# Kernel tuning notes

Hardware: AMD Instinct MI355X
Metric: run time of the kernel (lower is better)

The kernel has to match this reference:

```python
import jax, jax.numpy as jnp
import numpy as np

HOPS = 3  # max_hops; C has HOPS+1 tables

def setup_inputs() -> dict:
    key = jax.random.key(0)
    k1, k2, k3 = jax.random.split(key, 3)
    B, M, S, V, D = 32, 512, 10, 32000, 128
    story = jax.random.randint(k1, (B, M, S), 0, V)
    hidden = jax.random.normal(k2, (B, 1, D), dtype=jnp.float32)
    # hop+1 embedding tables, initialized N(0, 0.1) like the torch module
    C = 0.1 * jax.random.normal(k3, (HOPS + 1, V, D), dtype=jnp.float32)
    return {"story": story, "hidden": hidden, "C": C}

def reference(story, hidden, C):
    # story: [B, M, S] int tokens; hidden: [B, 1, D]; C: [HOPS+1, V, D]
    u = jnp.squeeze(hidden, axis=1)  # [B, D]
    prob_logit = None
    for h in range(HOPS):
        # embedding gather + bag-sum over sentence dim -> [B, M, D]
        embed_A = jnp.take(C[h], story, axis=0).sum(axis=2)
        # dot-product attention logits against current query u
        prob_logit = jnp.einsum('bmd,bd->bm', embed_A, u)  # [B, M]
        prob = jax.nn.softmax(prob_logit, axis=1)
        # second table gather + bag-sum, then softmax-weighted combine
        embed_C = jnp.take(C[h + 1], story, axis=0).sum(axis=2)  # [B, M, D]
        o_k = jnp.einsum('bm,bmd->bd', prob, embed_C)  # [B, D]
        u = u + o_k
    return prob_logit, u
```

## Files before the change

### kernel.cpp

```cpp
#include <hip/hip_runtime.h>

#define BB 32
#define MM 512
#define SS 10
#define VV 32000
#define DD 128
#define HOPS 3
#define BM (BB * MM)
#define NCHUNK 32
#define CHM (MM / NCHUNK)
#define PSTRIDE 132

__device__ __forceinline__ unsigned bfrn(float f) {
    unsigned u = __float_as_uint(f);
    return (u + 0x7FFFu + ((u >> 16) & 1u)) >> 16;
}
__device__ __forceinline__ float bflo(unsigned q) {
    return __uint_as_float(q << 16);
}
__device__ __forceinline__ float bfhi(unsigned q) {
    return __uint_as_float(q & 0xFFFF0000u);
}


__global__ __launch_bounds__(256) void cvt_bf16(const float* __restrict__ C,
                                                unsigned* __restrict__ Cb ) {
    const int gid = blockIdx.x * 256 + threadIdx.x;
    const float4 f0 = ((const float4*)C)[gid * 2];
    const float4 f1 = ((const float4*)C)[gid * 2 + 1];
    uint4 o;
    o.x = bfrn(f0.x) | (bfrn(f0.y) << 16);
    o.y = bfrn(f0.z) | (bfrn(f0.w) << 16);
    o.z = bfrn(f1.x) | (bfrn(f1.y) << 16);
    o.w = bfrn(f1.z) | (bfrn(f1.w) << 16);
    ((uint4*)Cb)[gid] = o;
}

template <int HOP>
__global__ __launch_bounds__(256) void hop_k(const int* __restrict__ story,
                                             const unsigned* __restrict__ Clog,
                                             const unsigned* __restrict__ Cout,
                                             const float* __restrict__ Elog,
                                             float* __restrict__ Eout,
                                             const float* __restrict__ uprev,
                                             const float* __restrict__ pin,
                                             const float* __restrict__ den_in_unused,
                                             float* __restrict__ uwrite,
                                             float* __restrict__ logit,
                                             float* __restrict__ pout) {
    const int b = blockIdx.y, c = blockIdx.x;
    const int tid = threadIdx.x;
    const int w = tid >> 6, lane = tid & 63;

    __shared__ float su[DD];
    if (tid < DD) {
        float v = uprev[b * DD + tid];
        if (HOP > 0) {
            float num = 0.f, dsum = 0.f;
            for (int cc = 0; cc < NCHUNK; ++cc) {
                const float* p = pin + ((size_t)b * NCHUNK + cc) * PSTRIDE;
                num += p[tid];
                dsum += p[DD];
            }
            v += num / dsum;
            if (c == 0) uwrite[b * DD + tid] = v;
        }
        su[tid] = v;
    }
    __syncthreads();
    const float2 uv = ((const float2*)su)[lane];

    float nx = 0.f, ny = 0.f, den = 0.f;
#pragma unroll
    for (int k = 0; k < CHM / 4; ++k) {
        const int m = c * CHM + k * 4 + w;
        const int bm = b * MM + m;
        int tok[SS];
        const int* st = story + (size_t)bm * SS;
#pragma unroll
        for (int s = 0; s < SS; ++s) tok[s] = st[s];

        float ex, ey;
        if (HOP == 0) {
            ex = 0.f; ey = 0.f;
#pragma unroll
            for (int s = 0; s < SS; ++s) {
                const unsigned q = (Clog + (size_t)tok[s] * (DD / 2))[lane];
                ex += bflo(q); ey += bfhi(q);
            }
        } else {
            const float2 v = ((const float2*)(Elog + (size_t)bm * DD))[lane];
            ex = v.x; ey = v.y;
        }
        float l = ex * uv.x + ey * uv.y;
#pragma unroll
        for (int off = 32; off; off >>= 1) l += __shfl_xor(l, off, 64);
        if (HOP == 2 && lane == 0) logit[bm] = l;
        const float e = expf(l);

        float rx = 0.f, ry = 0.f;
#pragma unroll
        for (int s = 0; s < SS; ++s) {
            const unsigned q = (Cout + (size_t)tok[s] * (DD / 2))[lane];
            rx += bflo(q); ry += bfhi(q);
        }
        if (HOP < 2)
            ((float2*)(Eout + (size_t)bm * DD))[lane] = make_float2(rx, ry);
        nx += e * rx; ny += e * ry; den += e;
    }

    __shared__ float sx[4][64], sy[4][64], sd[4];
    sx[w][lane] = nx; sy[w][lane] = ny;
    if (lane == 0) sd[w] = den;
    __syncthreads();
    if (w == 0) {
        const float ox = sx[0][lane] + sx[1][lane] + sx[2][lane] + sx[3][lane];
        const float oy = sy[0][lane] + sy[1][lane] + sy[2][lane] + sy[3][lane];
        float* prow = pout + ((size_t)b * NCHUNK + c) * PSTRIDE;
        ((float2*)prow)[lane] = make_float2(ox, oy);
        if (lane == 0) prow[DD] = sd[0] + sd[1] + sd[2] + sd[3];
    }
}

__global__ __launch_bounds__(128) void final_u(const float* __restrict__ pin,
                                               const float* __restrict__ u2,
                                               float* __restrict__ uout) {
    const int b = blockIdx.x, d = threadIdx.x;
    float num = 0.f, den = 0.f;
    for (int cc = 0; cc < NCHUNK; ++cc) {
        const float* p = pin + ((size_t)b * NCHUNK + cc) * PSTRIDE;
        num += p[d];
        den += p[DD];
    }
    uout[b * DD + d] = u2[b * DD + d] + num / den;
}

__global__ __launch_bounds__(256) void init_u(const float* __restrict__ hidden,
                                              float* __restrict__ u) {
    int i = blockIdx.x * 256 + threadIdx.x;
    if (i < BB * DD) u[i] = hidden[i];
}

__global__ __launch_bounds__(256) void logit_kernel(const int* __restrict__ story,
                                                    const float* __restrict__ Ch,
                                                    const float* __restrict__ u,
                                                    float* __restrict__ logit) {
    int wid = (blockIdx.x * 256 + threadIdx.x) >> 6;
    int lane = threadIdx.x & 63;
    if (wid >= BB * MM) return;
    int b = wid >> 9;
    const int* st = story + (size_t)wid * SS;
    int tok[SS];
#pragma unroll
    for (int s = 0; s < SS; ++s) tok[s] = st[s];
    float ax = 0.f, ay = 0.f;
#pragma unroll
    for (int s = 0; s < SS; ++s) {
        const float2 v = ((const float2*)(Ch + (size_t)tok[s] * DD))[lane];
        ax += v.x; ay += v.y;
    }
    const float2 uv = ((const float2*)(u + b * DD))[lane];
    float p = ax * uv.x + ay * uv.y;
#pragma unroll
    for (int off = 32; off; off >>= 1) p += __shfl_down(p, off, 64);
    if (lane == 0) logit[wid] = p;
}

__global__ __launch_bounds__(256) void softmax_kernel(const float* __restrict__ logit,
                                                      float* __restrict__ prob) {
    int b = blockIdx.x;
    int t = threadIdx.x;
    __shared__ float red[8];
    float l0 = logit[b * MM + t];
    float l1 = logit[b * MM + 256 + t];
    float mx = fmaxf(l0, l1);
#pragma unroll
    for (int off = 32; off; off >>= 1) mx = fmaxf(mx, __shfl_xor(mx, off, 64));
    if ((t & 63) == 0) red[t >> 6] = mx;
    __syncthreads();
    mx = fmaxf(fmaxf(red[0], red[1]), fmaxf(red[2], red[3]));
    float e0 = expf(l0 - mx), e1 = expf(l1 - mx);
    float s = e0 + e1;
#pragma unroll
    for (int off = 32; off; off >>= 1) s += __shfl_xor(s, off, 64);
    if ((t & 63) == 0) red[4 + (t >> 6)] = s;
    __syncthreads();
    s = red[4] + red[5] + red[6] + red[7];
    float inv = 1.0f / s;
    prob[b * MM + t] = e0 * inv;
    prob[b * MM + 256 + t] = e1 * inv;
}

__global__ __launch_bounds__(256) void partial_kernel(const int* __restrict__ story,
                                                      const float* __restrict__ Ch1,
                                                      const float* __restrict__ prob,
                                                      float* __restrict__ partial,
                                                      int chunk) {
    int b = blockIdx.y, c = blockIdx.x;
    int w = threadIdx.x >> 6, lane = threadIdx.x & 63;
    int m0 = c * chunk;
    float ax = 0.f, ay = 0.f;
    for (int m = m0 + w; m < m0 + chunk; m += 4) {
        float pw = prob[b * MM + m];
        const int* st = story + (size_t)(b * MM + m) * SS;
        int tok[SS];
#pragma unroll
        for (int s = 0; s < SS; ++s) tok[s] = st[s];
        float sx = 0.f, sy = 0.f;
#pragma unroll
        for (int s = 0; s < SS; ++s) {
            const float2 v = ((const float2*)(Ch1 + (size_t)tok[s] * DD))[lane];
            sx += v.x; sy += v.y;
        }
        ax += pw * sx; ay += pw * sy;
    }
    __shared__ float redx[4][64];
    __shared__ float redy[4][64];
    redx[w][lane] = ax;
    redy[w][lane] = ay;
    __syncthreads();
    if (w == 0) {
        float ox = redx[0][lane] + redx[1][lane] + redx[2][lane] + redx[3][lane];
        float oy = redy[0][lane] + redy[1][lane] + redy[2][lane] + redy[3][lane];
        float2* dst = (float2*)(partial + ((size_t)b * gridDim.x + c) * DD);
        dst[lane] = make_float2(ox, oy);
    }
}

__global__ __launch_bounds__(256) void update_kernel(const float* __restrict__ partial,
                                                     float* __restrict__ u, int NC) {
    int i = blockIdx.x * 256 + threadIdx.x;
    if (i >= BB * DD) return;
    int b = i >> 7, d = i & 127;
    float s = 0.f;
    for (int c = 0; c < NC; ++c) s += partial[((size_t)b * NC + c) * DD + d];
    u[i] += s;
}

extern "C" void kernel_launch(void* const* d_in, const int* in_sizes, int n_in,
                              void* d_out, int out_size, void* d_ws, size_t ws_size,
                              hipStream_t stream) {
    const int*   story  = (const int*)d_in[0];
    const float* hidden = (const float*)d_in[1];
    const float* Cmat   = (const float*)d_in[2];

    float* out   = (float*)d_out;
    float* logit = out;
    float* uout  = out + BB * MM;

    const size_t szCb = (size_t)4 * VV * DD / 2;
    const size_t szE  = (size_t)BM * DD;
    const size_t szP  = (size_t)BB * NCHUNK * PSTRIDE;
    const size_t need = (szCb + 2 * szE + 3 * szP + 2 * BB * DD) * sizeof(float);

    if (ws_size >= need) {
        unsigned* Cb = (unsigned*)d_ws;
        float* E1 = (float*)d_ws + szCb;
        float* E2 = E1 + szE;
        float* P0 = E2 + szE;
        float* P1 = P0 + szP;
        float* P2 = P1 + szP;
        float* u1 = P2 + szP;
        float* u2 = u1 + BB * DD;

        const unsigned* C0b = Cb;
        const unsigned* C1b = Cb + (size_t)1 * VV * DD / 2;
        const unsigned* C2b = Cb + (size_t)2 * VV * DD / 2;
        const unsigned* C3b = Cb + (size_t)3 * VV * DD / 2;

        cvt_bf16<<<(4 * VV * DD / 8) / 256, 256, 0, stream>>>(Cmat, Cb);

        hop_k<0><<<dim3(NCHUNK, BB), 256, 0, stream>>>(
            story, C0b, C1b, nullptr, E1, hidden, nullptr, nullptr, nullptr, nullptr, P0);
        hop_k<1><<<dim3(NCHUNK, BB), 256, 0, stream>>>(
            story, nullptr, C2b, E1, E2, hidden, P0, nullptr, u1, nullptr, P1);
        hop_k<2><<<dim3(NCHUNK, BB), 256, 0, stream>>>(
            story, nullptr, C3b, E2, nullptr, u1, P1, nullptr, u2, logit, P2);
        final_u<<<BB, 128, 0, stream>>>(P2, u2, uout);
    } else {
        float* prob = (float*)d_ws;
        int NC = 32;
        while (NC > 1 && (size_t)(BB * MM + BB * NC * DD) * 4 > ws_size) NC >>= 1;
        float* partial = prob + BB * MM;
        int chunk = MM / NC;

        init_u<<<(BB * DD + 255) / 256, 256, 0, stream>>>(hidden, uout);
        for (int h = 0; h < HOPS; ++h) {
            const float* Ca = Cmat + (size_t)h * VV * DD;
            const float* Cc = Cmat + (size_t)(h + 1) * VV * DD;
            logit_kernel<<<(BB * MM) / 4, 256, 0, stream>>>(story, Ca, uout, logit);
            softmax_kernel<<<BB, 256, 0, stream>>>(logit, prob);
            partial_kernel<<<dim3(NC, BB), 256, 0, stream>>>(story, Cc, prob, partial, chunk);
            update_kernel<<<(BB * DD + 255) / 256, 256, 0, stream>>>(partial, uout, NC);
        }
    }
}
```

Measured before the change: 66.10 us.

## Fuse conversion and all hops into one cooperative persistent kernel

Replaces the chain of separate kernel launches (bf16 conversion, three hop kernels, final reduction) with one cooperative persistent kernel that uses grid-wide syncs between stages. It also converts only tables C0 and C1 up front and converts C2 and C3 alongside hops 0 and 1, so conversion work overlaps with gather work. The goal is to remove launch gaps and tail idle time. In exchange it adds grid.sync costs and limits the grid to co-resident blocks, and it falls back to the old launch path if the cooperative launch fails.

```diff
diff --git a/kernel.cpp b/kernel.cpp
--- a/kernel.cpp
+++ b/kernel.cpp
@@ -1,4 +1,7 @@
 #include <hip/hip_runtime.h>
+#include <hip/hip_cooperative_groups.h>
+
+namespace cg = cooperative_groups;
 
 #define BB 32
 #define MM 512
@@ -8,24 +11,21 @@
 #define HOPS 3
 #define BM (BB * MM)
 #define NCHUNK 32
+#define NITEM (BB * NCHUNK)
 #define CHM (MM / NCHUNK)
 #define PSTRIDE 132
+#define GTHR 256
+#define UTAB ((size_t)VV * DD / 8)
 
 __device__ __forceinline__ unsigned bfrn(float f) {
     unsigned u = __float_as_uint(f);
     return (u + 0x7FFFu + ((u >> 16) & 1u)) >> 16;
 }
-__device__ __forceinline__ float bflo(unsigned q) {
-    return __uint_as_float(q << 16);
-}
-__device__ __forceinline__ float bfhi(unsigned q) {
-    return __uint_as_float(q & 0xFFFF0000u);
-}
-
-
-__global__ __launch_bounds__(256) void cvt_bf16(const float* __restrict__ C,
-                                                unsigned* __restrict__ Cb ) {
-    const int gid = blockIdx.x * 256 + threadIdx.x;
+__device__ __forceinline__ float bflo(unsigned q) { return __uint_as_float(q << 16); }
+__device__ __forceinline__ float bfhi(unsigned q) { return __uint_as_float(q & 0xFFFF0000u); }
+
+__device__ __forceinline__ void cvt_unit(const float* __restrict__ C,
+                                         unsigned* __restrict__ Cb, size_t gid) {
     const float4 f0 = ((const float4*)C)[gid * 2];
     const float4 f1 = ((const float4*)C)[gid * 2 + 1];
     uint4 o;
@@ -37,22 +37,21 @@
 }
 
 template <int HOP>
-__global__ __launch_bounds__(256) void hop_k(const int* __restrict__ story,
-                                             const unsigned* __restrict__ Clog,
-                                             const unsigned* __restrict__ Cout,
-                                             const float* __restrict__ Elog,
-                                             float* __restrict__ Eout,
-                                             const float* __restrict__ uprev,
-                                             const float* __restrict__ pin,
-                                             const float* __restrict__ den_in_unused,
-                                             float* __restrict__ uwrite,
-                                             float* __restrict__ logit,
-                                             float* __restrict__ pout) {
-    const int b = blockIdx.y, c = blockIdx.x;
-    const int tid = threadIdx.x;
+__device__ void hop_body(const int b, const int c, const int tid,
+                         const int* __restrict__ story,
+                         const unsigned* __restrict__ Clog,
+                         const unsigned* __restrict__ Cout,
+                         const float* __restrict__ Elog,
+                         float* __restrict__ Eout,
+                         const float* __restrict__ uprev,
+                         const float* __restrict__ pin,
+                         float* __restrict__ uwrite,
+                         float* __restrict__ logit,
+                         float* __restrict__ pout,
+                         float* __restrict__ su,
+                         float (*sx)[64], float (*sy)[64], float* sd) {
     const int w = tid >> 6, lane = tid & 63;
 
-    __shared__ float su[DD];
     if (tid < DD) {
         float v = uprev[b * DD + tid];
         if (HOP > 0) {
@@ -109,7 +108,7 @@
         nx += e * rx; ny += e * ry; den += e;
     }
 
-    __shared__ float sx[4][64], sy[4][64], sd[4];
+    __syncthreads();
     sx[w][lane] = nx; sy[w][lane] = ny;
     if (lane == 0) sd[w] = den;
     __syncthreads();
@@ -120,6 +119,94 @@
         ((float2*)prow)[lane] = make_float2(ox, oy);
         if (lane == 0) prow[DD] = sd[0] + sd[1] + sd[2] + sd[3];
     }
+}
+
+__global__ __launch_bounds__(GTHR, 2) void fused_all(const int* __restrict__ story,
+                                                     const float* __restrict__ hidden,
+                                                     const float* __restrict__ Cmat,
+                                                     unsigned* __restrict__ Cb,
+                                                     float* __restrict__ E1,
+                                                     float* __restrict__ E2,
+                                                     float* __restrict__ P0,
+                                                     float* __restrict__ P1,
+                                                     float* __restrict__ P2,
+                                                     float* __restrict__ u1,
+                                                     float* __restrict__ u2,
+                                                     float* __restrict__ logit,
+                                                     float* __restrict__ uout) {
+    cg::grid_group grid = cg::this_grid();
+    const int blk = blockIdx.x;
+    const int tid = threadIdx.x;
+    const int G = gridDim.x;
+    const size_t GS = (size_t)G * GTHR;
+
+    __shared__ float su[DD];
+    __shared__ float sx[4][64], sy[4][64];
+    __shared__ float sd[4];
+
+    const unsigned* C0b = Cb;
+    const unsigned* C1b = Cb + (size_t)1 * VV * DD / 2;
+    const unsigned* C2b = Cb + (size_t)2 * VV * DD / 2;
+    const unsigned* C3b = Cb + (size_t)3 * VV * DD / 2;
+
+    for (size_t g = (size_t)blk * GTHR + tid; g < 2 * UTAB; g += GS)
+        cvt_unit(Cmat, Cb, g);
+    grid.sync();
+
+    for (int item = blk; item < NITEM; item += G)
+        hop_body<0>(item >> 5, item & 31, tid, story, C0b, C1b, nullptr, E1,
+                    hidden, nullptr, nullptr, nullptr, P0, su, sx, sy, sd);
+    for (size_t g = (size_t)blk * GTHR + tid; g < UTAB; g += GS)
+        cvt_unit(Cmat, Cb, 2 * UTAB + g);
+    grid.sync();
+
+    for (int item = blk; item < NITEM; item += G)
+        hop_body<1>(item >> 5, item & 31, tid, story, nullptr, C2b, E1, E2,
+                    hidden, P0, u1, nullptr, P1, su, sx, sy, sd);
+    for (size_t g = (size_t)blk * GTHR + tid; g < UTAB; g += GS)
+        cvt_unit(Cmat, Cb, 3 * UTAB + g);
+    grid.sync();
+
+    for (int item = blk; item < NITEM; item += G)
+        hop_body<2>(item >> 5, item & 31, tid, story, nullptr, C3b, E2, nullptr,
+                    u1, P1, u2, logit, P2, su, sx, sy, sd);
+    grid.sync();
+
+    for (int item = blk; item < 16; item += G) {
+        const int i = item * GTHR + tid;
+        const int bb = i >> 7, d = i & 127;
+        float num = 0.f, dsum = 0.f;
+        for (int cc = 0; cc < NCHUNK; ++cc) {
+            const float* p = P2 + ((size_t)bb * NCHUNK + cc) * PSTRIDE;
+            num += p[d];
+            dsum += p[DD];
+        }
+        uout[bb * DD + d] = u2[bb * DD + d] + num / dsum;
+    }
+}
+
+__global__ __launch_bounds__(256) void cvt_bf16(const float* __restrict__ C,
+                                                unsigned* __restrict__ Cb) {
+    const int gid = blockIdx.x * 256 + threadIdx.x;
+    cvt_unit(C, Cb, (size_t)gid);
+}
+
+template <int HOP>
+__global__ __launch_bounds__(256) void hop_k(const int* __restrict__ story,
+                                             const unsigned* __restrict__ Clog,
+                                             const unsigned* __restrict__ Cout,
+                                             const float* __restrict__ Elog,
+                                             float* __restrict__ Eout,
+                                             const float* __restrict__ uprev,
+                                             const float* __restrict__ pin,
+                                             float* __restrict__ uwrite,
+                                             float* __restrict__ logit,
+                                             float* __restrict__ pout) {
+    __shared__ float su[DD];
+    __shared__ float sx[4][64], sy[4][64];
+    __shared__ float sd[4];
+    hop_body<HOP>(blockIdx.y, blockIdx.x, threadIdx.x, story, Clog, Cout, Elog,
+                  Eout, uprev, pin, uwrite, logit, pout, su, sx, sy, sd);
 }
 
 __global__ __launch_bounds__(128) void final_u(const float* __restrict__ pin,
@@ -268,15 +355,41 @@
         const unsigned* C2b = Cb + (size_t)2 * VV * DD / 2;
         const unsigned* C3b = Cb + (size_t)3 * VV * DD / 2;
 
-        cvt_bf16<<<(4 * VV * DD / 8) / 256, 256, 0, stream>>>(Cmat, Cb);
-
-        hop_k<0><<<dim3(NCHUNK, BB), 256, 0, stream>>>(
-            story, C0b, C1b, nullptr, E1, hidden, nullptr, nullptr, nullptr, nullptr, P0);
-        hop_k<1><<<dim3(NCHUNK, BB), 256, 0, stream>>>(
-            story, nullptr, C2b, E1, E2, hidden, P0, nullptr, u1, nullptr, P1);
-        hop_k<2><<<dim3(NCHUNK, BB), 256, 0, stream>>>(
-            story, nullptr, C3b, E2, nullptr, u1, P1, nullptr, u2, logit, P2);
-        final_u<<<BB, 128, 0, stream>>>(P2, u2, uout);
+        bool coop_done = false;
+        int maxActive = 0;
+        if (hipOccupancyMaxActiveBlocksPerMultiprocessor(&maxActive, fused_all,
+                                                         GTHR, 0) == hipSuccess &&
+            maxActive > 0) {
+            hipDeviceProp_t prop;
+            int dev = 0;
+            hipGetDevice(&dev);
+            if (hipGetDeviceProperties(&prop, dev) == hipSuccess) {
+                int grid = maxActive * prop.multiProcessorCount;
+                if (grid > NITEM) grid = NITEM;
+                if (grid >= 256) {
+                    void* args[] = {(void*)&story, (void*)&hidden, (void*)&Cmat,
+                                    (void*)&Cb, (void*)&E1, (void*)&E2,
+                                    (void*)&P0, (void*)&P1, (void*)&P2,
+                                    (void*)&u1, (void*)&u2, (void*)&logit,
+                                    (void*)&uout};
+                    if (hipLaunchCooperativeKernel((void*)fused_all, dim3(grid),
+                                                   dim3(GTHR), args, 0,
+                                                   stream) == hipSuccess)
+                        coop_done = true;
+                }
+            }
+        }
+
+        if (!coop_done) {
+            cvt_bf16<<<(4 * VV * DD / 8) / 256, 256, 0, stream>>>(Cmat, Cb);
+            hop_k<0><<<dim3(NCHUNK, BB), 256, 0, stream>>>(
+                story, C0b, C1b, nullptr, E1, hidden, nullptr, nullptr, nullptr, P0);
+            hop_k<1><<<dim3(NCHUNK, BB), 256, 0, stream>>>(
+                story, nullptr, C2b, E1, E2, hidden, P0, u1, nullptr, P1);
+            hop_k<2><<<dim3(NCHUNK, BB), 256, 0, stream>>>(
+                story, nullptr, C3b, E2, nullptr, u1, P1, u2, logit, P2);
+            final_u<<<BB, 128, 0, stream>>>(P2, u2, uout);
+        }
     } else {
         float* prob = (float*)d_ws;
         int NC = 32;
```

Result: slower. 249.9 us (+278.0%).

## Overlap bf16 table conversion with hop kernels and double chunk count

Applied to the files above, without the earlier changes.

The upfront bf16 conversion now covers only tables 0 and 1. Tables 2 and 3 are converted at the tail of the hop 0 and hop 1 kernels, each one just before the hop that reads it. This hides part of the conversion traffic behind the gather work. NCHUNK goes from 32 to 64, which doubles the grid and leaves each block fewer rows. Two partial buffers are reused in ping-pong fashion, at the cost of more partial-sum reduction work per hop.

```diff
diff --git a/kernel.cpp b/kernel.cpp
--- a/kernel.cpp
+++ b/kernel.cpp
@@ -7,25 +7,20 @@
 #define DD 128
 #define HOPS 3
 #define BM (BB * MM)
-#define NCHUNK 32
+#define NCHUNK 64
 #define CHM (MM / NCHUNK)
 #define PSTRIDE 132
+#define UTAB ((size_t)VV * DD / 8)
 
 __device__ __forceinline__ unsigned bfrn(float f) {
     unsigned u = __float_as_uint(f);
     return (u + 0x7FFFu + ((u >> 16) & 1u)) >> 16;
 }
-__device__ __forceinline__ float bflo(unsigned q) {
-    return __uint_as_float(q << 16);
-}
-__device__ __forceinline__ float bfhi(unsigned q) {
-    return __uint_as_float(q & 0xFFFF0000u);
-}
-
-
-__global__ __launch_bounds__(256) void cvt_bf16(const float* __restrict__ C,
-                                                unsigned* __restrict__ Cb ) {
-    const int gid = blockIdx.x * 256 + threadIdx.x;
+__device__ __forceinline__ float bflo(unsigned q) { return __uint_as_float(q << 16); }
+__device__ __forceinline__ float bfhi(unsigned q) { return __uint_as_float(q & 0xFFFF0000u); }
+
+__device__ __forceinline__ void cvt_unit(const float* __restrict__ C,
+                                         unsigned* __restrict__ Cb, size_t gid) {
     const float4 f0 = ((const float4*)C)[gid * 2];
     const float4 f1 = ((const float4*)C)[gid * 2 + 1];
     uint4 o;
@@ -37,22 +32,21 @@
 }
 
 template <int HOP>
-__global__ __launch_bounds__(256) void hop_k(const int* __restrict__ story,
-                                             const unsigned* __restrict__ Clog,
-                                             const unsigned* __restrict__ Cout,
-                                             const float* __restrict__ Elog,
-                                             float* __restrict__ Eout,
-                                             const float* __restrict__ uprev,
-                                             const float* __restrict__ pin,
-                                             const float* __restrict__ den_in_unused,
-                                             float* __restrict__ uwrite,
-                                             float* __restrict__ logit,
-                                             float* __restrict__ pout) {
-    const int b = blockIdx.y, c = blockIdx.x;
-    const int tid = threadIdx.x;
+__device__ void hop_body(const int b, const int c, const int tid,
+                         const int* __restrict__ story,
+                         const unsigned* __restrict__ Clog,
+                         const unsigned* __restrict__ Cout,
+                         const float* __restrict__ Elog,
+                         float* __restrict__ Eout,
+                         const float* __restrict__ uprev,
+                         const float* __restrict__ pin,
+                         float* __restrict__ uwrite,
+                         float* __restrict__ logit,
+                         float* __restrict__ pout,
+                         float* __restrict__ su,
+                         float (*sx)[64], float (*sy)[64], float* sd) {
     const int w = tid >> 6, lane = tid & 63;
 
-    __shared__ float su[DD];
     if (tid < DD) {
         float v = uprev[b * DD + tid];
         if (HOP > 0) {
@@ -109,7 +103,6 @@
         nx += e * rx; ny += e * ry; den += e;
     }
 
-    __shared__ float sx[4][64], sy[4][64], sd[4];
     sx[w][lane] = nx; sy[w][lane] = ny;
     if (lane == 0) sd[w] = den;
     __syncthreads();
@@ -119,6 +112,39 @@
         float* prow = pout + ((size_t)b * NCHUNK + c) * PSTRIDE;
         ((float2*)prow)[lane] = make_float2(ox, oy);
         if (lane == 0) prow[DD] = sd[0] + sd[1] + sd[2] + sd[3];
+    }
+}
+
+
+__global__ __launch_bounds__(256) void cvt01(const float* __restrict__ C,
+                                             unsigned* __restrict__ Cb) {
+    const size_t g = (size_t)blockIdx.x * 256 + threadIdx.x;
+    if (g < 2 * UTAB) cvt_unit(C, Cb, g);
+}
+
+template <int HOP, int CVT>
+__global__ __launch_bounds__(256) void hop_k(const int* __restrict__ story,
+                                             const unsigned* __restrict__ Clog,
+                                             const unsigned* __restrict__ Cout,
+                                             const float* __restrict__ Elog,
+                                             float* __restrict__ Eout,
+                                             const float* __restrict__ uprev,
+                                             const float* __restrict__ pin,
+                                             float* __restrict__ uwrite,
+                                             float* __restrict__ logit,
+                                             float* __restrict__ pout,
+                                             const float* __restrict__ Cmat,
+                                             unsigned* __restrict__ Cb,
+                                             size_t cvt_base) {
+    __shared__ float su[DD];
+    __shared__ float sx[4][64], sy[4][64];
+    __shared__ float sd[4];
+    hop_body<HOP>(blockIdx.y, blockIdx.x, threadIdx.x, story, Clog, Cout, Elog,
+                  Eout, uprev, pin, uwrite, logit, pout, su, sx, sy, sd);
+    if (CVT) {
+        const size_t blk = (size_t)blockIdx.y * gridDim.x + blockIdx.x;
+        const size_t g = blk * 256 + threadIdx.x;
+        if (g < UTAB) cvt_unit(Cmat, Cb, cvt_base + g);
     }
 }
 
@@ -251,16 +277,15 @@
     const size_t szCb = (size_t)4 * VV * DD / 2;
     const size_t szE  = (size_t)BM * DD;
     const size_t szP  = (size_t)BB * NCHUNK * PSTRIDE;
-    const size_t need = (szCb + 2 * szE + 3 * szP + 2 * BB * DD) * sizeof(float);
+    const size_t need = (szCb + 2 * szE + 2 * szP + 2 * BB * DD) * sizeof(float);
 
     if (ws_size >= need) {
         unsigned* Cb = (unsigned*)d_ws;
         float* E1 = (float*)d_ws + szCb;
         float* E2 = E1 + szE;
-        float* P0 = E2 + szE;
-        float* P1 = P0 + szP;
-        float* P2 = P1 + szP;
-        float* u1 = P2 + szP;
+        float* Pa = E2 + szE;
+        float* Pb = Pa + szP;
+        float* u1 = Pb + szP;
         float* u2 = u1 + BB * DD;
 
         const unsigned* C0b = Cb;
@@ -268,15 +293,17 @@
         const unsigned* C2b = Cb + (size_t)2 * VV * DD / 2;
         const unsigned* C3b = Cb + (size_t)3 * VV * DD / 2;
 
-        cvt_bf16<<<(4 * VV * DD / 8) / 256, 256, 0, stream>>>(Cmat, Cb);
-
-        hop_k<0><<<dim3(NCHUNK, BB), 256, 0, stream>>>(
-            story, C0b, C1b, nullptr, E1, hidden, nullptr, nullptr, nullptr, nullptr, P0);
-        hop_k<1><<<dim3(NCHUNK, BB), 256, 0, stream>>>(
-            story, nullptr, C2b, E1, E2, hidden, P0, nullptr, u1, nullptr, P1);
-        hop_k<2><<<dim3(NCHUNK, BB), 256, 0, stream>>>(
-            story, nullptr, C3b, E2, nullptr, u1, P1, nullptr, u2, logit, P2);
-        final_u<<<BB, 128, 0, stream>>>(P2, u2, uout);
+        cvt01<<<(unsigned)((2 * UTAB + 255) / 256), 256, 0, stream>>>(Cmat, Cb);
+        hop_k<0, 1><<<dim3(NCHUNK, BB), 256, 0, stream>>>(
+            story, C0b, C1b, nullptr, E1, hidden, nullptr, nullptr, nullptr, Pa,
+            Cmat, Cb, 2 * UTAB);
+        hop_k<1, 1><<<dim3(NCHUNK, BB), 256, 0, stream>>>(
+            story, nullptr, C2b, E1, E2, hidden, Pa, u1, nullptr, Pb,
+            Cmat, Cb, 3 * UTAB);
+        hop_k<2, 0><<<dim3(NCHUNK, BB), 256, 0, stream>>>(
+            story, nullptr, C3b, E2, nullptr, u1, Pb, u2, logit, Pa,
+            nullptr, nullptr, 0);
+        final_u<<<BB, 128, 0, stream>>>(Pa, u2, uout);
     } else {
         float* prob = (float*)d_ws;
         int NC = 32;
```

Result: no change. 66.15 us (+0.1%).

## Interleave bf16 table pairs and fuse gathers across hops, overlap conversion

Applied to the files above, without the earlier changes.

Converts embedding tables into interleaved pairs (C0/C1, C2/C3) so one 8-byte gather per token fetches both tables. Hop 0 reads C0 and C1 together, and hop 1 reads C2 and C3 and precomputes E3. That lets hop 2 skip token gathers and read only precomputed sums. Conversion of C2/C3 moves into the hop-0 kernel tail so it overlaps with gather work instead of running as a separate full-table pass up front. The cost is an extra E3 buffer write and read.

```diff
diff --git a/kernel.cpp b/kernel.cpp
--- a/kernel.cpp
+++ b/kernel.cpp
@@ -10,52 +10,46 @@
 #define NCHUNK 32
 #define CHM (MM / NCHUNK)
 #define PSTRIDE 132
+#define PAIR_UNITS ((size_t)VV * 32)
 
 __device__ __forceinline__ unsigned bfrn(float f) {
     unsigned u = __float_as_uint(f);
     return (u + 0x7FFFu + ((u >> 16) & 1u)) >> 16;
 }
-__device__ __forceinline__ float bflo(unsigned q) {
-    return __uint_as_float(q << 16);
-}
-__device__ __forceinline__ float bfhi(unsigned q) {
-    return __uint_as_float(q & 0xFFFF0000u);
-}
-
-
-__global__ __launch_bounds__(256) void cvt_bf16(const float* __restrict__ C,
-                                                unsigned* __restrict__ Cb ) {
-    const int gid = blockIdx.x * 256 + threadIdx.x;
-    const float4 f0 = ((const float4*)C)[gid * 2];
-    const float4 f1 = ((const float4*)C)[gid * 2 + 1];
+__device__ __forceinline__ unsigned pk(float a, float b) { return bfrn(a) | (bfrn(b) << 16); }
+__device__ __forceinline__ float bflo(unsigned q) { return __uint_as_float(q << 16); }
+__device__ __forceinline__ float bfhi(unsigned q) { return __uint_as_float(q & 0xFFFF0000u); }
+
+__device__ __forceinline__ void cvt_pair_unit(const float* __restrict__ CA,
+                                              const float* __restrict__ CB,
+                                              unsigned* __restrict__ dst, size_t g) {
+    const size_t v = g >> 5, j = g & 31;
+    const float4 a = ((const float4*)CA)[v * 32 + j];
+    const float4 b = ((const float4*)CB)[v * 32 + j];
     uint4 o;
-    o.x = bfrn(f0.x) | (bfrn(f0.y) << 16);
-    o.y = bfrn(f0.z) | (bfrn(f0.w) << 16);
-    o.z = bfrn(f1.x) | (bfrn(f1.y) << 16);
-    o.w = bfrn(f1.z) | (bfrn(f1.w) << 16);
-    ((uint4*)Cb)[gid] = o;
-}
-
-template <int HOP>
-__global__ __launch_bounds__(256) void hop_k(const int* __restrict__ story,
-                                             const unsigned* __restrict__ Clog,
-                                             const unsigned* __restrict__ Cout,
-                                             const float* __restrict__ Elog,
-                                             float* __restrict__ Eout,
-                                             const float* __restrict__ uprev,
-                                             const float* __restrict__ pin,
-                                             const float* __restrict__ den_in_unused,
-                                             float* __restrict__ uwrite,
-                                             float* __restrict__ logit,
-                                             float* __restrict__ pout) {
-    const int b = blockIdx.y, c = blockIdx.x;
-    const int tid = threadIdx.x;
-    const int w = tid >> 6, lane = tid & 63;
-
-    __shared__ float su[DD];
+    o.x = pk(a.x, a.y);
+    o.y = pk(b.x, b.y);
+    o.z = pk(a.z, a.w);
+    o.w = pk(b.z, b.w);
+    ((uint4*)dst)[v * 32 + j] = o;
+}
+
+
+__global__ __launch_bounds__(256) void cvt01(const float* __restrict__ Cmat,
+                                             unsigned* __restrict__ Cb01) {
+    const size_t g = (size_t)blockIdx.x * 256 + threadIdx.x;
+    if (g < PAIR_UNITS)
+        cvt_pair_unit(Cmat, Cmat + (size_t)VV * DD, Cb01, g);
+}
+
+__device__ __forceinline__ void stage_u(const int b, const int c, const int tid,
+                                        const float* __restrict__ uprev,
+                                        const float* __restrict__ pin,
+                                        float* __restrict__ uwrite,
+                                        float* __restrict__ su) {
     if (tid < DD) {
         float v = uprev[b * DD + tid];
-        if (HOP > 0) {
+        if (pin) {
             float num = 0.f, dsum = 0.f;
             for (int cc = 0; cc < NCHUNK; ++cc) {
                 const float* p = pin + ((size_t)b * NCHUNK + cc) * PSTRIDE;
@@ -63,53 +57,19 @@
                 dsum += p[DD];
             }
             v += num / dsum;
-            if (c == 0) uwrite[b * DD + tid] = v;
+            if (c == 0 && uwrite) uwrite[b * DD + tid] = v;
         }
         su[tid] = v;
     }
     __syncthreads();
-    const float2 uv = ((const float2*)su)[lane];
-
-    float nx = 0.f, ny = 0.f, den = 0.f;
-#pragma unroll
-    for (int k = 0; k < CHM / 4; ++k) {
-        const int m = c * CHM + k * 4 + w;
-        const int bm = b * MM + m;
-        int tok[SS];
-        const int* st = story + (size_t)bm * SS;
-#pragma unroll
-        for (int s = 0; s < SS; ++s) tok[s] = st[s];
-
-        float ex, ey;
-        if (HOP == 0) {
-            ex = 0.f; ey = 0.f;
-#pragma unroll
-            for (int s = 0; s < SS; ++s) {
-                const unsigned q = (Clog + (size_t)tok[s] * (DD / 2))[lane];
-                ex += bflo(q); ey += bfhi(q);
-            }
-        } else {
-            const float2 v = ((const float2*)(Elog + (size_t)bm * DD))[lane];
-            ex = v.x; ey = v.y;
-        }
-        float l = ex * uv.x + ey * uv.y;
-#pragma unroll
-        for (int off = 32; off; off >>= 1) l += __shfl_xor(l, off, 64);
-        if (HOP == 2 && lane == 0) logit[bm] = l;
-        const float e = expf(l);
-
-        float rx = 0.f, ry = 0.f;
-#pragma unroll
-        for (int s = 0; s < SS; ++s) {
-            const unsigned q = (Cout + (size_t)tok[s] * (DD / 2))[lane];
-            rx += bflo(q); ry += bfhi(q);
-        }
-        if (HOP < 2)
-            ((float2*)(Eout + (size_t)bm * DD))[lane] = make_float2(rx, ry);
-        nx += e * rx; ny += e * ry; den += e;
-    }
-
-    __shared__ float sx[4][64], sy[4][64], sd[4];
+}
+
+__device__ __forceinline__ void write_partial(const int b, const int c,
+                                              const int w, const int lane,
+                                              float nx, float ny, float den,
+                                              float* __restrict__ pout,
+                                              float (*sx)[64], float (*sy)[64],
+                                              float* sd) {
     sx[w][lane] = nx; sy[w][lane] = ny;
     if (lane == 0) sd[w] = den;
     __syncthreads();
@@ -120,6 +80,147 @@
         ((float2*)prow)[lane] = make_float2(ox, oy);
         if (lane == 0) prow[DD] = sd[0] + sd[1] + sd[2] + sd[3];
     }
+}
+
+__global__ __launch_bounds__(256) void hop0_k(const int* __restrict__ story,
+                                              const unsigned* __restrict__ Cb01,
+                                              float* __restrict__ E1,
+                                              const float* __restrict__ hidden,
+                                              float* __restrict__ pout,
+                                              const float* __restrict__ Cmat,
+                                              unsigned* __restrict__ Cb23) {
+    const int b = blockIdx.y, c = blockIdx.x;
+    const int tid = threadIdx.x;
+    const int w = tid >> 6, lane = tid & 63;
+    __shared__ float su[DD];
+    __shared__ float sx[4][64], sy[4][64];
+    __shared__ float sd[4];
+
+    stage_u(b, c, tid, hidden, nullptr, nullptr, su);
+    const float2 uv = ((const float2*)su)[lane];
+    const uint2* G = (const uint2*)Cb01;
+
+    float nx = 0.f, ny = 0.f, den = 0.f;
+#pragma unroll
+    for (int k = 0; k < CHM / 4; ++k) {
+        const int m = c * CHM + k * 4 + w;
+        const int bm = b * MM + m;
+        int tok[SS];
+        const int* st = story + (size_t)bm * SS;
+#pragma unroll
+        for (int s = 0; s < SS; ++s) tok[s] = st[s];
+
+        float ex = 0.f, ey = 0.f, rx = 0.f, ry = 0.f;
+#pragma unroll
+        for (int s = 0; s < SS; ++s) {
+            const uint2 q = G[(size_t)tok[s] * 64 + lane];
+            ex += bflo(q.x); ey += bfhi(q.x);
+            rx += bflo(q.y); ry += bfhi(q.y);
+        }
+        float l = ex * uv.x + ey * uv.y;
+#pragma unroll
+        for (int off = 32; off; off >>= 1) l += __shfl_xor(l, off, 64);
+        const float e = expf(l);
+
+        ((float2*)(E1 + (size_t)bm * DD))[lane] = make_float2(rx, ry);
+        nx += e * rx; ny += e * ry; den += e;
+    }
+    write_partial(b, c, w, lane, nx, ny, den, pout, sx, sy, sd);
+
+    const size_t t0 = (((size_t)blockIdx.y * gridDim.x + blockIdx.x) * 256 + tid) * 4;
+#pragma unroll
+    for (int i = 0; i < 4; ++i) {
+        const size_t g = t0 + i;
+        if (g < PAIR_UNITS)
+            cvt_pair_unit(Cmat + (size_t)2 * VV * DD, Cmat + (size_t)3 * VV * DD,
+                          Cb23, g);
+    }
+}
+
+__global__ __launch_bounds__(256) void hop1_k(const int* __restrict__ story,
+                                              const unsigned* __restrict__ Cb23,
+                                              const float* __restrict__ E1,
+                                              float* __restrict__ E2,
+                                              float* __restrict__ E3,
+                                              const float* __restrict__ hidden,
+                                              const float* __restrict__ pin,
+                                              float* __restrict__ u1,
+                                              float* __restrict__ pout) {
+    const int b = blockIdx.y, c = blockIdx.x;
+    const int tid = threadIdx.x;
+    const int w = tid >> 6, lane = tid & 63;
+    __shared__ float su[DD];
+    __shared__ float sx[4][64], sy[4][64];
+    __shared__ float sd[4];
+
+    stage_u(b, c, tid, hidden, pin, u1, su);
+    const float2 uv = ((const float2*)su)[lane];
+    const uint2* G = (const uint2*)Cb23;
+
+    float nx = 0.f, ny = 0.f, den = 0.f;
+#pragma unroll
+    for (int k = 0; k < CHM / 4; ++k) {
+        const int m = c * CHM + k * 4 + w;
+        const int bm = b * MM + m;
+        int tok[SS];
+        const int* st = story + (size_t)bm * SS;
+#pragma unroll
+        for (int s = 0; s < SS; ++s) tok[s] = st[s];
+
+        const float2 ev = ((const float2*)(E1 + (size_t)bm * DD))[lane];
+        float l = ev.x * uv.x + ev.y * uv.y;
+#pragma unroll
+        for (int off = 32; off; off >>= 1) l += __shfl_xor(l, off, 64);
+        const float e = expf(l);
+
+        float r2x = 0.f, r2y = 0.f, r3x = 0.f, r3y = 0.f;
+#pragma unroll
+        for (int s = 0; s < SS; ++s) {
+            const uint2 q = G[(size_t)tok[s] * 64 + lane];
+            r2x += bflo(q.x); r2y += bfhi(q.x);
+            r3x += bflo(q.y); r3y += bfhi(q.y);
+        }
+        ((float2*)(E2 + (size_t)bm * DD))[lane] = make_float2(r2x, r2y);
+        ((float2*)(E3 + (size_t)bm * DD))[lane] = make_float2(r3x, r3y);
+        nx += e * r2x; ny += e * r2y; den += e;
+    }
+    write_partial(b, c, w, lane, nx, ny, den, pout, sx, sy, sd);
+}
+
+__global__ __launch_bounds__(256) void hop2_k(const float* __restrict__ E2,
+                                              const float* __restrict__ E3,
+                                              const float* __restrict__ u1,
+                                              const float* __restrict__ pin,
+                                              float* __restrict__ u2,
+                                              float* __restrict__ logit,
+                                              float* __restrict__ pout) {
+    const int b = blockIdx.y, c = blockIdx.x;
+    const int tid = threadIdx.x;
+    const int w = tid >> 6, lane = tid & 63;
+    __shared__ float su[DD];
+    __shared__ float sx[4][64], sy[4][64];
+    __shared__ float sd[4];
+
+    stage_u(b, c, tid, u1, pin, u2, su);
+    const float2 uv = ((const float2*)su)[lane];
+
+    float nx = 0.f, ny = 0.f, den = 0.f;
+#pragma unroll
+    for (int k = 0; k < CHM / 4; ++k) {
+        const int m = c * CHM + k * 4 + w;
+        const int bm = b * MM + m;
+
+        const float2 ev = ((const float2*)(E2 + (size_t)bm * DD))[lane];
+        float l = ev.x * uv.x + ev.y * uv.y;
+#pragma unroll
+        for (int off = 32; off; off >>= 1) l += __shfl_xor(l, off, 64);
+        if (lane == 0) logit[bm] = l;
+        const float e = expf(l);
+
+        const float2 rv = ((const float2*)(E3 + (size_t)bm * DD))[lane];
+        nx += e * rv.x; ny += e * rv.y; den += e;
+    }
+    write_partial(b, c, w, lane, nx, ny, den, pout, sx, sy, sd);
 }
 
 __global__ __launch_bounds__(128) void final_u(const float* __restrict__ pin,
@@ -248,35 +349,29 @@
     float* logit = out;
     float* uout  = out + BB * MM;
 
-    const size_t szCb = (size_t)4 * VV * DD / 2;
-    const size_t szE  = (size_t)BM * DD;
-    const size_t szP  = (size_t)BB * NCHUNK * PSTRIDE;
-    const size_t need = (szCb + 2 * szE + 3 * szP + 2 * BB * DD) * sizeof(float);
+    const size_t szCbp = (size_t)VV * 128;
+    const size_t szE   = (size_t)BM * DD;
+    const size_t szP   = (size_t)BB * NCHUNK * PSTRIDE;
+    const size_t need  = (2 * szCbp + 3 * szE + 2 * szP + 2 * BB * DD) * sizeof(float);
 
     if (ws_size >= need) {
-        unsigned* Cb = (unsigned*)d_ws;
-        float* E1 = (float*)d_ws + szCb;
+        unsigned* Cb01 = (unsigned*)d_ws;
+        unsigned* Cb23 = Cb01 + szCbp;
+        float* E1 = (float*)d_ws + 2 * szCbp;
         float* E2 = E1 + szE;
-        float* P0 = E2 + szE;
-        float* P1 = P0 + szP;
-        float* P2 = P1 + szP;
-        float* u1 = P2 + szP;
+        float* E3 = E2 + szE;
+        float* Pa = E3 + szE;
+        float* Pb = Pa + szP;
+        float* u1 = Pb + szP;
         float* u2 = u1 + BB * DD;
 
-        const unsigned* C0b = Cb;
-        const unsigned* C1b = Cb + (size_t)1 * VV * DD / 2;
-        const unsigned* C2b = Cb + (size_t)2 * VV * DD / 2;
-        const unsigned* C3b = Cb + (size_t)3 * VV * DD / 2;
-
-        cvt_bf16<<<(4 * VV * DD / 8) / 256, 256, 0, stream>>>(Cmat, Cb);
-
-        hop_k<0><<<dim3(NCHUNK, BB), 256, 0, stream>>>(
-            story, C0b, C1b, nullptr, E1, hidden, nullptr, nullptr, nullptr, nullptr, P0);
-        hop_k<1><<<dim3(NCHUNK, BB), 256, 0, stream>>>(
-            story, nullptr, C2b, E1, E2, hidden, P0, nullptr, u1, nullptr, P1);
-        hop_k<2><<<dim3(NCHUNK, BB), 256, 0, stream>>>(
-            story, nullptr, C3b, E2, nullptr, u1, P1, nullptr, u2, logit, P2);
-        final_u<<<BB, 128, 0, stream>>>(P2, u2, uout);
+        cvt01<<<(unsigned)((PAIR_UNITS + 255) / 256), 256, 0, stream>>>(Cmat, Cb01);
+        hop0_k<<<dim3(NCHUNK, BB), 256, 0, stream>>>(story, Cb01, E1, hidden, Pa,
+                                                     Cmat, Cb23);
+        hop1_k<<<dim3(NCHUNK, BB), 256, 0, stream>>>(story, Cb23, E1, E2, E3,
+                                                     hidden, Pa, u1, Pb);
+        hop2_k<<<dim3(NCHUNK, BB), 256, 0, stream>>>(E2, E3, u1, Pb, u2, logit, Pa);
+        final_u<<<BB, 128, 0, stream>>>(Pa, u2, uout);
     } else {
         float* prob = (float*)d_ws;
         int NC = 32;
```

After: 65.12 us. About the same (-1.5%).
